# Kernel optimization log

Hardware: AMD Instinct MI355X
Metric: run time of the kernel (lower is better)

Reference implementation:

```python
import jax, jax.numpy as jnp
import numpy as np
import math

SIZE = 2048
N_CLASSES = 16
STEPS = 100
DT = 0.03
GAMMA = 0.125
BETA = 1.0
EIG = 1.0
EPSILON = 0.1


def _make_P(size=SIZE, n_classes=N_CLASSES):
    # Default attractor construction: block indicator columns.
    attr = np.zeros((size, n_classes), dtype=np.float32)
    block = size // n_classes
    for c in range(n_classes):
        attr[c * block:(c + 1) * block, c] = 1.0
    norm_attr = attr / (np.linalg.norm(attr, axis=0, keepdims=True) + 1e-8) ** 2
    return jnp.asarray(norm_attr @ attr.T)  # [size, size] projection onto attractor subspace


def setup_inputs() -> dict:
    key = jax.random.key(0)
    kx, ka, kg, kn = jax.random.split(key, 4)
    x = jax.random.normal(kx, (512, SIZE), dtype=jnp.float32)
    # kaiming_uniform_(a=sqrt(5)) => U(-1/sqrt(fan_in), 1/sqrt(fan_in))
    bound = 1.0 / math.sqrt(SIZE)
    A = jax.random.uniform(ka, (SIZE, SIZE), minval=-bound, maxval=bound, dtype=jnp.float32)
    G = jax.random.uniform(kg, (SIZE, SIZE), minval=-bound, maxval=bound, dtype=jnp.float32)
    noise = jax.random.normal(kn, (STEPS, 512, SIZE), dtype=jnp.float32)
    return {"x": x, "A": A, "G": G, "noise": noise}


def reference(x, A, G, noise):
    P = _make_P()
    antiP = jnp.eye(SIZE, dtype=x.dtype) - P
    B = (A @ antiP + EIG * P).T  # [size, size]
    GT = G.T
    sqrt_dt = math.sqrt(DT)

    def nl(x):
        x2 = x * x
        return x2 / (GAMMA + x2)

    def step(x, n):
        x_dot = -x + BETA * (nl(x) @ B)
        x_new = x + DT * x_dot + sqrt_dt * EPSILON * (n @ GT)
        return x_new, None

    x_final, _ = jax.lax.scan(step, x, noise)
    return x_final
```

## Files before the change

### kernel.cpp

```cpp
#include <hip/hip_runtime.h>
#include <cstdint>


typedef unsigned short ushort_t;
typedef __bf16 bf16x8 __attribute__((ext_vector_type(8)));
typedef float f32x4 __attribute__((ext_vector_type(4)));
typedef unsigned short u16x4 __attribute__((ext_vector_type(4)));
typedef unsigned short u16x8 __attribute__((ext_vector_type(8)));

#define SZ 2048
#define BATCH 512
#define NSTEPS 100

static constexpr float DT = 0.03f;
static constexpr float GAM = 0.125f;
static constexpr float PVAL = (float)(1.0 / (128.0 + 2.2627416997969522e-07));
static constexpr float CNOISE = 0.017320508075688773f;

__device__ __forceinline__ unsigned short f2bf(float f) {
    unsigned int u = __builtin_bit_cast(unsigned int, f);
    return (unsigned short)((u + 0x7fffu + ((u >> 16) & 1u)) >> 16);
}

__device__ __forceinline__ void async16(const void* g, void* l) {
    __builtin_amdgcn_global_load_lds(
        (__attribute__((address_space(1))) void*)(uintptr_t)g,
        (__attribute__((address_space(3))) void*)(uint32_t)(uintptr_t)l,
        16, 0, 0);
}

__global__ __launch_bounds__(256) void prep_kernel(const float* __restrict__ A,
                                                   const float* __restrict__ G,
                                                   ushort_t* __restrict__ BTs,
                                                   ushort_t* __restrict__ Gs) {
    const int n = blockIdx.x;
    const int t = threadIdx.x;
    __shared__ float s16[16];
    const float* arow = A + (size_t)n * SZ;
    f32x4 a0 = *(const f32x4*)(arow + t * 8);
    f32x4 a1 = *(const f32x4*)(arow + t * 8 + 4);
    float ps = a0[0] + a0[1] + a0[2] + a0[3] + a1[0] + a1[1] + a1[2] + a1[3];
#pragma unroll
    for (int m = 1; m < 16; m <<= 1) ps += __shfl_xor(ps, m, 64);
    if ((t & 15) == 0) s16[t >> 4] = ps * PVAL;
    __syncthreads();
    const int seg = t >> 4;
    const float s = s16[seg];
    const float diag = (seg == (n >> 7)) ? PVAL : 0.0f;
    float av[8] = {a0[0], a0[1], a0[2], a0[3], a1[0], a1[1], a1[2], a1[3]};
    u16x8 ov;
#pragma unroll
    for (int i = 0; i < 8; ++i) ov[i] = f2bf(DT * (av[i] - s + diag));
    *(u16x8*)&BTs[(size_t)n * SZ + t * 8] = ov;

    const float* grow = G + (size_t)n * SZ;
    f32x4 g0 = *(const f32x4*)(grow + t * 8);
    f32x4 g1 = *(const f32x4*)(grow + t * 8 + 4);
    float gv[8] = {g0[0], g0[1], g0[2], g0[3], g1[0], g1[1], g1[2], g1[3]};
    u16x8 og;
#pragma unroll
    for (int i = 0; i < 8; ++i) og[i] = f2bf(CNOISE * gv[i]);
    *(u16x8*)&Gs[(size_t)n * SZ + t * 8] = og;
}

__global__ __launch_bounds__(256) void init_kernel(const float* __restrict__ x,
                                                   const float* __restrict__ noise,
                                                   float* __restrict__ xbuf,
                                                   ushort_t* __restrict__ Y0,
                                                   ushort_t* __restrict__ N0) {
    const size_t i = ((size_t)blockIdx.x * 256 + threadIdx.x) * 4;
    const size_t NX = (size_t)BATCH * SZ;
    if (i < NX) {
        f32x4 xv = *(const f32x4*)(x + i);
        *(f32x4*)(xbuf + i) = xv;
        u16x4 yv;
#pragma unroll
        for (int e = 0; e < 4; ++e) {
            float x2 = xv[e] * xv[e];
            yv[e] = f2bf(x2 / (GAM + x2));
        }
        *(u16x4*)(Y0 + i) = yv;
    } else {
        size_t j = i - NX;
        f32x4 nv = *(const f32x4*)(noise + j);
        u16x4 nb;
#pragma unroll
        for (int e = 0; e < 4; ++e) nb[e] = f2bf(nv[e]);
        *(u16x4*)(N0 + j) = nb;
    }
}

__global__ __launch_bounds__(256) void step_kernel(
    const ushort_t* __restrict__ Ycur, const ushort_t* __restrict__ Ncur,
    const ushort_t* __restrict__ BTs, const ushort_t* __restrict__ Gs,
    const float* xin, float* xout,
    ushort_t* __restrict__ Ynext, const float* __restrict__ noise_next,
    ushort_t* __restrict__ Nnext, int do_noise) {
    extern __shared__ ushort_t smem[];
    const int tid = threadIdx.x;
    const int w = tid >> 6;
    const int l = tid & 63;
    const int m0 = blockIdx.y << 6;
    const int n0 = blockIdx.x << 6;

    const char* Ag;
    const char* Bg;
    {
        const ushort_t* As;
        const ushort_t* Bs;
        int kb0;
        if (w < 2) { As = Ycur; Bs = BTs; kb0 = w * 2048; }
        else       { As = Ncur; Bs = Gs;  kb0 = (w - 2) * 2048; }
        Ag = (const char*)As + (size_t)m0 * 4096 + kb0;
        Bg = (const char*)Bs + (size_t)n0 * 4096 + kb0;
    }
    ushort_t* waveLds = smem + w * 16384;

    const int srow = l >> 3;
    const int sq = (l & 7) ^ srow;
    const int sgo = srow * 4096 + sq * 16;

    f32x4 acc[4][4] = {};

    auto stage = [&](int ci, int b) {
        const char* Ac = Ag + ci * 128;
        const char* Bc = Bg + ci * 128;
        ushort_t* dA = waveLds + b * 8192;
        ushort_t* dB = dA + 4096;
#pragma unroll
        for (int i = 0; i < 8; ++i) {
            async16(Ac + i * 32768 + sgo, dA + i * 512);
            async16(Bc + i * 32768 + sgo, dB + i * 512);
        }
    };

    const int lr = l & 15;
    const int q8 = l >> 4;
    const int swz = lr & 7;

    auto compute = [&](int b) {
        const char* TA = (const char*)waveLds + b * 16384;
        const char* TB = TA + 8192;
#pragma unroll
        for (int half = 0; half < 2; ++half) {
            const int qpos = ((((half << 2) | q8) ^ swz) << 4);
            bf16x8 af[4], bfv[4];
#pragma unroll
            for (int f = 0; f < 4; ++f) {
                const int rowb = (f * 16 + lr) * 128;
                af[f] = *(const bf16x8*)(TA + rowb + qpos);
                bfv[f] = *(const bf16x8*)(TB + rowb + qpos);
            }
#pragma unroll
            for (int fr = 0; fr < 4; ++fr)
#pragma unroll
                for (int fc = 0; fc < 4; ++fc)
                    acc[fr][fc] = __builtin_amdgcn_mfma_f32_16x16x32_bf16(
                        af[fr], bfv[fc], acc[fr][fc], 0, 0, 0);
        }
    };

    stage(0, 0);
#pragma unroll 2
    for (int ci = 0; ci < 16; ++ci) {
        if (ci < 15) {
            stage(ci + 1, (ci + 1) & 1);
            asm volatile("s_waitcnt vmcnt(16)" ::: "memory");
        } else {
            asm volatile("s_waitcnt vmcnt(0)" ::: "memory");
        }
        compute(ci & 1);
    }

    __syncthreads();
    float* redF = (float*)smem;
    {
        const int base = w * 4352;
#pragma unroll
        for (int fr = 0; fr < 4; ++fr)
#pragma unroll
            for (int fc = 0; fc < 4; ++fc) {
                const int c = fc * 16 + lr;
                const int rb = fr * 16 + q8 * 4;
#pragma unroll
                for (int reg = 0; reg < 4; ++reg)
                    redF[base + (rb + reg) * 68 + c] = acc[fr][fc][reg];
            }
    }
    __syncthreads();
    {
        const int r = tid >> 2;
        const int c0 = (tid & 3) << 4;
        const size_t gb = (size_t)(m0 + r) * SZ + n0 + c0;
#pragma unroll
        for (int j = 0; j < 4; ++j) {
            f32x4 s = *(const f32x4*)&redF[0 * 4352 + r * 68 + c0 + j * 4];
            s = s + *(const f32x4*)&redF[1 * 4352 + r * 68 + c0 + j * 4];
            s = s + *(const f32x4*)&redF[2 * 4352 + r * 68 + c0 + j * 4];
            s = s + *(const f32x4*)&redF[3 * 4352 + r * 68 + c0 + j * 4];
            f32x4 xv = *(const f32x4*)(xin + gb + j * 4);
            f32x4 xn = xv * (1.0f - DT) + s;
            *(f32x4*)(xout + gb + j * 4) = xn;
            u16x4 yv;
#pragma unroll
            for (int e = 0; e < 4; ++e) {
                float x2 = xn[e] * xn[e];
                yv[e] = f2bf(x2 / (GAM + x2));
            }
            *(u16x4*)(Ynext + gb + j * 4) = yv;
        }
        if (do_noise) {
#pragma unroll
            for (int j = 0; j < 4; ++j) {
                f32x4 nv = *(const f32x4*)(noise_next + gb + j * 4);
                u16x4 nb;
#pragma unroll
                for (int e = 0; e < 4; ++e) nb[e] = f2bf(nv[e]);
                *(u16x4*)(Nnext + gb + j * 4) = nb;
            }
        }
    }
}

extern "C" void kernel_launch(void* const* d_in, const int* in_sizes, int n_in,
                              void* d_out, int out_size, void* d_ws, size_t ws_size,
                              hipStream_t stream) {
    const float* x = (const float*)d_in[0];
    const float* A = (const float*)d_in[1];
    const float* G = (const float*)d_in[2];
    const float* noise = (const float*)d_in[3];
    float* out = (float*)d_out;
    char* ws = (char*)d_ws;

    float* xbuf = (float*)(ws);
    ushort_t* Y0 = (ushort_t*)(ws + (4u << 20));
    ushort_t* Y1 = (ushort_t*)(ws + (6u << 20));
    ushort_t* N0 = (ushort_t*)(ws + (8u << 20));
    ushort_t* N1 = (ushort_t*)(ws + (10u << 20));
    ushort_t* BTs = (ushort_t*)(ws + (12u << 20));
    ushort_t* Gsc = (ushort_t*)(ws + (20u << 20));

    (void)hipFuncSetAttribute((const void*)step_kernel,
                              hipFuncAttributeMaxDynamicSharedMemorySize, 131072);

    prep_kernel<<<dim3(SZ), dim3(256), 0, stream>>>(A, G, BTs, Gsc);
    init_kernel<<<dim3(2048), dim3(256), 0, stream>>>(x, noise, xbuf, Y0, N0);

    ushort_t* Yc = Y0;
    ushort_t* Yn = Y1;
    ushort_t* Nc = N0;
    ushort_t* Nn = N1;
    for (int t = 0; t < NSTEPS; ++t) {
        float* xo = (t == NSTEPS - 1) ? out : xbuf;
        const int dn = (t < NSTEPS - 1) ? 1 : 0;
        const float* nnext = noise + (size_t)(t + 1) * BATCH * SZ;
        step_kernel<<<dim3(32, 8), dim3(256), 131072, stream>>>(
            Yc, Nc, BTs, Gsc, xbuf, xo, Yn, dn ? nnext : noise, Nn, dn);
        ushort_t* tmp = Yc; Yc = Yn; Yn = tmp;
        tmp = Nc; Nc = Nn; Nn = tmp;
    }
}
```

Measured before the change: 2.219 ms.

## Precompute all noise projections in one batched GEMM outside the sequential loop

The noise term n@G^T does not depend on x, so all 100 steps' noise projections are computed up front by one large GEMM (51200x2048x2048) into a bf16 buffer Z. Each step kernel then only does the Y@B GEMM, with K split across 8 waves per 512-thread block, and adds the precomputed Z slice in the epilogue. This halves the serial per-step GEMM work and fills the GPU with one big parallel GEMM, but adds a ~200MB bf16 workspace and rounds the noise contribution to bf16 after the product.

```diff
diff --git a/kernel.cpp b/kernel.cpp
--- a/kernel.cpp
+++ b/kernel.cpp
@@ -21,12 +21,25 @@
     unsigned int u = __builtin_bit_cast(unsigned int, f);
     return (unsigned short)((u + 0x7fffu + ((u >> 16) & 1u)) >> 16);
 }
-
+__device__ __forceinline__ float bf2f(unsigned short h) {
+    unsigned int u = ((unsigned int)h) << 16;
+    return __builtin_bit_cast(float, u);
+}
 __device__ __forceinline__ void async16(const void* g, void* l) {
     __builtin_amdgcn_global_load_lds(
         (__attribute__((address_space(1))) void*)(uintptr_t)g,
         (__attribute__((address_space(3))) void*)(uint32_t)(uintptr_t)l,
         16, 0, 0);
+}
+
+__global__ __launch_bounds__(256) void conv_kernel(const float* __restrict__ n,
+                                                   ushort_t* __restrict__ nb) {
+    const size_t i = ((size_t)blockIdx.x * 256 + threadIdx.x) * 4;
+    f32x4 v = *(const f32x4*)(n + i);
+    u16x4 o;
+#pragma unroll
+    for (int e = 0; e < 4; ++e) o[e] = f2bf(v[e]);
+    *(u16x4*)(nb + i) = o;
 }
 
 __global__ __launch_bounds__(256) void prep_kernel(const float* __restrict__ A,
@@ -64,92 +77,57 @@
 }
 
 __global__ __launch_bounds__(256) void init_kernel(const float* __restrict__ x,
-                                                   const float* __restrict__ noise,
                                                    float* __restrict__ xbuf,
-                                                   ushort_t* __restrict__ Y0,
-                                                   ushort_t* __restrict__ N0) {
+                                                   ushort_t* __restrict__ Y0) {
     const size_t i = ((size_t)blockIdx.x * 256 + threadIdx.x) * 4;
-    const size_t NX = (size_t)BATCH * SZ;
-    if (i < NX) {
-        f32x4 xv = *(const f32x4*)(x + i);
-        *(f32x4*)(xbuf + i) = xv;
-        u16x4 yv;
-#pragma unroll
-        for (int e = 0; e < 4; ++e) {
-            float x2 = xv[e] * xv[e];
-            yv[e] = f2bf(x2 / (GAM + x2));
-        }
-        *(u16x4*)(Y0 + i) = yv;
-    } else {
-        size_t j = i - NX;
-        f32x4 nv = *(const f32x4*)(noise + j);
-        u16x4 nb;
-#pragma unroll
-        for (int e = 0; e < 4; ++e) nb[e] = f2bf(nv[e]);
-        *(u16x4*)(N0 + j) = nb;
-    }
-}
-
-__global__ __launch_bounds__(256) void step_kernel(
-    const ushort_t* __restrict__ Ycur, const ushort_t* __restrict__ Ncur,
-    const ushort_t* __restrict__ BTs, const ushort_t* __restrict__ Gs,
-    const float* xin, float* xout,
-    ushort_t* __restrict__ Ynext, const float* __restrict__ noise_next,
-    ushort_t* __restrict__ Nnext, int do_noise) {
-    extern __shared__ ushort_t smem[];
+    f32x4 xv = *(const f32x4*)(x + i);
+    *(f32x4*)(xbuf + i) = xv;
+    u16x4 yv;
+#pragma unroll
+    for (int e = 0; e < 4; ++e) {
+        float x2 = xv[e] * xv[e];
+        yv[e] = f2bf(x2 / (GAM + x2));
+    }
+    *(u16x4*)(Y0 + i) = yv;
+}
+
+__global__ __launch_bounds__(256) void zgemm_kernel(const ushort_t* __restrict__ Nb,
+                                                    const ushort_t* __restrict__ Gs,
+                                                    ushort_t* __restrict__ Z) {
+    __shared__ ushort_t sm[16384];
     const int tid = threadIdx.x;
-    const int w = tid >> 6;
-    const int l = tid & 63;
-    const int m0 = blockIdx.y << 6;
-    const int n0 = blockIdx.x << 6;
-
-    const char* Ag;
-    const char* Bg;
-    {
-        const ushort_t* As;
-        const ushort_t* Bs;
-        int kb0;
-        if (w < 2) { As = Ycur; Bs = BTs; kb0 = w * 2048; }
-        else       { As = Ncur; Bs = Gs;  kb0 = (w - 2) * 2048; }
-        Ag = (const char*)As + (size_t)m0 * 4096 + kb0;
-        Bg = (const char*)Bs + (size_t)n0 * 4096 + kb0;
-    }
-    ushort_t* waveLds = smem + w * 16384;
-
-    const int srow = l >> 3;
-    const int sq = (l & 7) ^ srow;
-    const int sgo = srow * 4096 + sq * 16;
-
+    const int w = tid >> 6, l = tid & 63;
+    const int m0 = blockIdx.y << 7, n0 = blockIdx.x << 7;
+    const char* Ag = (const char*)Nb + (size_t)m0 * 4096;
+    const char* Bg = (const char*)Gs + (size_t)n0 * 4096;
+    const int goff = (tid >> 3) * 4096 + (((tid & 7) ^ ((tid >> 3) & 7)) << 4);
+    const int loff = tid * 16;
+    const int lr = l & 15, q8 = l >> 4;
+    const int wm = (w & 1) << 6, wn = (w >> 1) << 6;
+    const int swz = lr & 7;
     f32x4 acc[4][4] = {};
 
-    auto stage = [&](int ci, int b) {
-        const char* Ac = Ag + ci * 128;
-        const char* Bc = Bg + ci * 128;
-        ushort_t* dA = waveLds + b * 8192;
-        ushort_t* dB = dA + 4096;
-#pragma unroll
-        for (int i = 0; i < 8; ++i) {
-            async16(Ac + i * 32768 + sgo, dA + i * 512);
-            async16(Bc + i * 32768 + sgo, dB + i * 512);
-        }
-    };
-
-    const int lr = l & 15;
-    const int q8 = l >> 4;
-    const int swz = lr & 7;
-
-    auto compute = [&](int b) {
-        const char* TA = (const char*)waveLds + b * 16384;
-        const char* TB = TA + 8192;
+    char* sA = (char*)sm;
+    char* sB = sA + 16384;
+    for (int kk = 0; kk < 32; ++kk) {
+        __syncthreads();
+        const char* Ac = Ag + kk * 128;
+        const char* Bc = Bg + kk * 128;
+#pragma unroll
+        for (int i = 0; i < 4; ++i) {
+            async16(Ac + i * 131072 + goff, sA + i * 4096 + loff);
+            async16(Bc + i * 131072 + goff, sB + i * 4096 + loff);
+        }
+        asm volatile("s_waitcnt vmcnt(0)" ::: "memory");
+        __syncthreads();
 #pragma unroll
         for (int half = 0; half < 2; ++half) {
             const int qpos = ((((half << 2) | q8) ^ swz) << 4);
             bf16x8 af[4], bfv[4];
 #pragma unroll
             for (int f = 0; f < 4; ++f) {
-                const int rowb = (f * 16 + lr) * 128;
-                af[f] = *(const bf16x8*)(TA + rowb + qpos);
-                bfv[f] = *(const bf16x8*)(TB + rowb + qpos);
+                af[f] = *(const bf16x8*)(sA + (wm + f * 16 + lr) * 128 + qpos);
+                bfv[f] = *(const bf16x8*)(sB + (wn + f * 16 + lr) * 128 + qpos);
             }
 #pragma unroll
             for (int fr = 0; fr < 4; ++fr)
@@ -158,66 +136,119 @@
                     acc[fr][fc] = __builtin_amdgcn_mfma_f32_16x16x32_bf16(
                         af[fr], bfv[fc], acc[fr][fc], 0, 0, 0);
         }
+    }
+    ushort_t* zr = Z + (size_t)m0 * SZ + n0;
+#pragma unroll
+    for (int fr = 0; fr < 4; ++fr)
+#pragma unroll
+        for (int reg = 0; reg < 4; ++reg) {
+            const size_t rb = (size_t)(wm + fr * 16 + q8 * 4 + reg) * SZ;
+#pragma unroll
+            for (int fc = 0; fc < 4; ++fc)
+                zr[rb + wn + fc * 16 + lr] = f2bf(acc[fr][fc][reg]);
+        }
+}
+
+__global__ __launch_bounds__(512, 2) void step_kernel(
+    const ushort_t* __restrict__ Ycur, const ushort_t* __restrict__ BTs,
+    const ushort_t* __restrict__ Zt, const float* __restrict__ xin,
+    float* __restrict__ xout, ushort_t* __restrict__ Ynext) {
+    extern __shared__ ushort_t smem[];
+    const int tid = threadIdx.x;
+    const int w = tid >> 6, l = tid & 63;
+    const int m0 = blockIdx.y << 6, n0 = blockIdx.x << 6;
+
+    const char* Ag = (const char*)Ycur + (size_t)m0 * 4096 + w * 512;
+    const char* Bg = (const char*)BTs + (size_t)n0 * 4096 + w * 512;
+    char* waveLds = (char*)smem + w * 16384;
+
+    const int goffL = (l >> 2) * 4096 + ((((l & 3) ^ ((l >> 3) & 3))) << 4);
+    const int loffL = l * 16;
+    const int lr = l & 15, q8 = l >> 4;
+    const int swz2 = (lr >> 1) & 3;
+
+    f32x4 acc[4][4] = {};
+
+    auto stage = [&](int ci, int b) {
+        const char* Ac = Ag + ci * 64;
+        const char* Bc = Bg + ci * 64;
+        char* dA = waveLds + b * 8192;
+        char* dB = dA + 4096;
+#pragma unroll
+        for (int i = 0; i < 4; ++i) {
+            async16(Ac + i * 65536 + goffL, dA + i * 1024 + loffL);
+            async16(Bc + i * 65536 + goffL, dB + i * 1024 + loffL);
+        }
+    };
+    auto compute = [&](int b) {
+        const char* TA = waveLds + b * 8192;
+        const char* TB = TA + 4096;
+        const int qpos = ((q8 ^ swz2) << 4);
+        bf16x8 af[4], bfv[4];
+#pragma unroll
+        for (int f = 0; f < 4; ++f) {
+            af[f] = *(const bf16x8*)(TA + (f * 16 + lr) * 64 + qpos);
+            bfv[f] = *(const bf16x8*)(TB + (f * 16 + lr) * 64 + qpos);
+        }
+#pragma unroll
+        for (int fr = 0; fr < 4; ++fr)
+#pragma unroll
+            for (int fc = 0; fc < 4; ++fc)
+                acc[fr][fc] = __builtin_amdgcn_mfma_f32_16x16x32_bf16(
+                    af[fr], bfv[fc], acc[fr][fc], 0, 0, 0);
     };
 
     stage(0, 0);
 #pragma unroll 2
-    for (int ci = 0; ci < 16; ++ci) {
-        if (ci < 15) {
+    for (int ci = 0; ci < 8; ++ci) {
+        if (ci < 7) {
             stage(ci + 1, (ci + 1) & 1);
-            asm volatile("s_waitcnt vmcnt(16)" ::: "memory");
+            asm volatile("s_waitcnt vmcnt(8)" ::: "memory");
         } else {
             asm volatile("s_waitcnt vmcnt(0)" ::: "memory");
         }
         compute(ci & 1);
     }
 
-    __syncthreads();
     float* redF = (float*)smem;
-    {
-        const int base = w * 4352;
-#pragma unroll
-        for (int fr = 0; fr < 4; ++fr)
+#pragma unroll
+    for (int p = 0; p < 2; ++p) {
+        __syncthreads();
+#pragma unroll
+        for (int fl = 0; fl < 2; ++fl) {
+            const int fr = p * 2 + fl;
+            const int rl = fl * 16 + q8 * 4;
 #pragma unroll
             for (int fc = 0; fc < 4; ++fc) {
                 const int c = fc * 16 + lr;
-                const int rb = fr * 16 + q8 * 4;
 #pragma unroll
                 for (int reg = 0; reg < 4; ++reg)
-                    redF[base + (rb + reg) * 68 + c] = acc[fr][fc][reg];
+                    redF[w * 2176 + (rl + reg) * 68 + c] = acc[fr][fc][reg];
             }
-    }
-    __syncthreads();
-    {
-        const int r = tid >> 2;
-        const int c0 = (tid & 3) << 4;
-        const size_t gb = (size_t)(m0 + r) * SZ + n0 + c0;
-#pragma unroll
-        for (int j = 0; j < 4; ++j) {
-            f32x4 s = *(const f32x4*)&redF[0 * 4352 + r * 68 + c0 + j * 4];
-            s = s + *(const f32x4*)&redF[1 * 4352 + r * 68 + c0 + j * 4];
-            s = s + *(const f32x4*)&redF[2 * 4352 + r * 68 + c0 + j * 4];
-            s = s + *(const f32x4*)&redF[3 * 4352 + r * 68 + c0 + j * 4];
-            f32x4 xv = *(const f32x4*)(xin + gb + j * 4);
-            f32x4 xn = xv * (1.0f - DT) + s;
-            *(f32x4*)(xout + gb + j * 4) = xn;
+        }
+        __syncthreads();
+        {
+            const int r = tid >> 4;
+            const int c0 = (tid & 15) << 2;
+            const int off = r * 68 + c0;
+            f32x4 s = *(const f32x4*)&redF[off];
+#pragma unroll
+            for (int ww = 1; ww < 8; ++ww)
+                s = s + *(const f32x4*)&redF[ww * 2176 + off];
+            const size_t gb = (size_t)(m0 + p * 32 + r) * SZ + n0 + c0;
+            f32x4 xv = *(const f32x4*)(xin + gb);
+            u16x4 zb = *(const u16x4*)(Zt + gb);
+            f32x4 xn;
+#pragma unroll
+            for (int e = 0; e < 4; ++e) xn[e] = xv[e] * (1.0f - DT) + s[e] + bf2f(zb[e]);
+            *(f32x4*)(xout + gb) = xn;
             u16x4 yv;
 #pragma unroll
             for (int e = 0; e < 4; ++e) {
                 float x2 = xn[e] * xn[e];
                 yv[e] = f2bf(x2 / (GAM + x2));
             }
-            *(u16x4*)(Ynext + gb + j * 4) = yv;
-        }
-        if (do_noise) {
-#pragma unroll
-            for (int j = 0; j < 4; ++j) {
-                f32x4 nv = *(const f32x4*)(noise_next + gb + j * 4);
-                u16x4 nb;
-#pragma unroll
-                for (int e = 0; e < 4; ++e) nb[e] = f2bf(nv[e]);
-                *(u16x4*)(Nnext + gb + j * 4) = nb;
-            }
+            *(u16x4*)(Ynext + gb) = yv;
         }
     }
 }
@@ -233,30 +264,27 @@
     char* ws = (char*)d_ws;
 
     float* xbuf = (float*)(ws);
-    ushort_t* Y0 = (ushort_t*)(ws + (4u << 20));
-    ushort_t* Y1 = (ushort_t*)(ws + (6u << 20));
-    ushort_t* N0 = (ushort_t*)(ws + (8u << 20));
-    ushort_t* N1 = (ushort_t*)(ws + (10u << 20));
-    ushort_t* BTs = (ushort_t*)(ws + (12u << 20));
-    ushort_t* Gsc = (ushort_t*)(ws + (20u << 20));
+    ushort_t* Y0 = (ushort_t*)(ws + ((size_t)4 << 20));
+    ushort_t* Y1 = (ushort_t*)(ws + ((size_t)6 << 20));
+    ushort_t* BTs = (ushort_t*)(ws + ((size_t)8 << 20));
+    ushort_t* Gsc = (ushort_t*)(ws + ((size_t)16 << 20));
+    ushort_t* Nb = (ushort_t*)(ws + ((size_t)24 << 20));
+    ushort_t* Z = (ushort_t*)(ws + ((size_t)240 << 20));
 
     (void)hipFuncSetAttribute((const void*)step_kernel,
                               hipFuncAttributeMaxDynamicSharedMemorySize, 131072);
 
+    conv_kernel<<<dim3(102400), dim3(256), 0, stream>>>(noise, Nb);
     prep_kernel<<<dim3(SZ), dim3(256), 0, stream>>>(A, G, BTs, Gsc);
-    init_kernel<<<dim3(2048), dim3(256), 0, stream>>>(x, noise, xbuf, Y0, N0);
+    init_kernel<<<dim3(1024), dim3(256), 0, stream>>>(x, xbuf, Y0);
+    zgemm_kernel<<<dim3(16, 400), dim3(256), 0, stream>>>(Nb, Gsc, Z);
 
     ushort_t* Yc = Y0;
     ushort_t* Yn = Y1;
-    ushort_t* Nc = N0;
-    ushort_t* Nn = N1;
     for (int t = 0; t < NSTEPS; ++t) {
         float* xo = (t == NSTEPS - 1) ? out : xbuf;
-        const int dn = (t < NSTEPS - 1) ? 1 : 0;
-        const float* nnext = noise + (size_t)(t + 1) * BATCH * SZ;
-        step_kernel<<<dim3(32, 8), dim3(256), 131072, stream>>>(
-            Yc, Nc, BTs, Gsc, xbuf, xo, Yn, dn ? nnext : noise, Nn, dn);
+        step_kernel<<<dim3(32, 8), dim3(512), 131072, stream>>>(
+            Yc, BTs, Z + (size_t)t * BATCH * SZ, xbuf, xo, Yn);
         ushort_t* tmp = Yc; Yc = Yn; Yn = tmp;
-        tmp = Nc; Nc = Nn; Nn = tmp;
-    }
-}
+    }
+}
```

Result: slower. 2.770 ms (+24.8%).
